# Performance work log

Hardware: AMD Instinct MI355X
Metric: run time of the kernel (lower is better)

The kernel has to match this reference:

```python
import jax, jax.numpy as jnp
import numpy as np

NR_EMB = 1024
B_COMMITMENT = 1.0


def setup_inputs() -> dict:
    key = jax.random.key(0)
    k1, k2 = jax.random.split(key)
    inpt = jax.random.normal(k1, (64, 2048, 64), dtype=jnp.float32)
    # VarianceScaling(uniform) over shape (D, K): limit = sqrt(3*scale/fan_in), scale=1, fan_in=D
    D = 64
    limit = np.sqrt(3.0 / D).astype(np.float32)
    emb_mtrx = jax.random.uniform(k2, (D, NR_EMB), dtype=jnp.float32, minval=-limit, maxval=limit)
    return {"inpt": inpt, "emb_mtrx": emb_mtrx}


def reference(inpt, emb_mtrx):
    D = inpt.shape[-1]
    x = inpt.reshape(-1, D)  # [N, D]
    dist = (jnp.sum(x * x, axis=1, keepdims=True)
            - 2.0 * (x @ emb_mtrx)
            + jnp.sum(emb_mtrx * emb_mtrx, axis=0, keepdims=True))
    idx = jnp.argmax(-dist, axis=1)  # [N]
    # avg_probs = mean of one-hot over N == normalized histogram (same math, no N x K one-hot)
    avg_probs = jnp.bincount(idx, length=NR_EMB).astype(inpt.dtype) / x.shape[0]
    perplexity = jnp.exp(-jnp.sum(avg_probs * jnp.log(avg_probs + 1e-10)))
    idx_nd = idx.reshape(inpt.shape[:-1])  # [B, T]
    q = jnp.take(emb_mtrx.T, idx_nd, axis=0)  # gather codebook rows -> [B, T, D]
    l_commitment = jnp.mean((jax.lax.stop_gradient(q) - inpt) ** 2)
    l_codebook = jnp.mean((q - jax.lax.stop_gradient(inpt)) ** 2)
    loss = B_COMMITMENT * l_commitment + l_codebook
    q = inpt + jax.lax.stop_gradient(q - inpt)  # straight-through estimator
    return q, loss, perplexity
```

## Files before the change

### kernel.cpp

```cpp
#include <hip/hip_runtime.h>

#define NROWS 131072
#define D 64
#define K 1024

typedef __attribute__((ext_vector_type(8))) short short8;
typedef __attribute__((ext_vector_type(4))) float f32x4;


__device__ __forceinline__ unsigned short f2bf(float f) {
    unsigned u = __float_as_uint(f);
    u += 0x7fff + ((u >> 16) & 1);
    return (unsigned short)(u >> 16);
}

__global__ __launch_bounds__(256) void prep_kernel(const float* __restrict__ E,
                                                   unsigned short* __restrict__ ehT,
                                                   float* __restrict__ eTf,
                                                   float* __restrict__ e2p,
                                                   int* __restrict__ hist) {
    const int k = (blockIdx.x & 3) * 256 + threadIdx.x;
    const int dq = blockIdx.x >> 2;
    float f[16];
    float s = 0.f;
#pragma unroll
    for (int j = 0; j < 16; ++j) {
        float v = E[(dq * 16 + j) * K + k];
        f[j] = v;
        s = fmaf(v, v, s);
    }
    short8 h0, h1;
#pragma unroll
    for (int j = 0; j < 8; ++j) {
        h0[j] = (short)f2bf(f[j]);
        h1[j] = (short)f2bf(f[8 + j]);
    }
    *(short8*)(ehT + (size_t)k * D + dq * 16) = h0;
    *(short8*)(ehT + (size_t)k * D + dq * 16 + 8) = h1;
#pragma unroll
    for (int c = 0; c < 4; ++c) {
        float4 v = {f[c * 4], f[c * 4 + 1], f[c * 4 + 2], f[c * 4 + 3]};
        *(float4*)(eTf + (size_t)k * D + dq * 16 + c * 4) = v;
    }
    e2p[dq * K + k] = s;
    if (dq == 0) hist[k] = 0;
}

__global__ __launch_bounds__(256, 4) void score_kernel(const float* __restrict__ X,
                                                       const unsigned short* __restrict__ ehT,
                                                       const float* __restrict__ e2p,
                                                       const float* __restrict__ eTf,
                                                       int* __restrict__ hist,
                                                       float* __restrict__ wavesum,
                                                       float* __restrict__ q) {
    __shared__ unsigned short ehs[256 * 64];
    __shared__ float e2s[256];
    __shared__ int idxs[4][32];

    const int wave = threadIdx.x >> 6;
    const int lane = threadIdx.x & 63;
    const int quad = lane >> 4;
    const int lc = lane & 15;
    const size_t row0 = (size_t)blockIdx.x * 128 + wave * 32;

    short8 ax[2][2];
#pragma unroll
    for (int s = 0; s < 2; ++s) {
        const float* xr = X + (row0 + s * 16 + lc) * D;
#pragma unroll
        for (int ks = 0; ks < 2; ++ks) {
            float4 a = *(const float4*)(xr + ks * 32 + quad * 8);
            float4 b = *(const float4*)(xr + ks * 32 + quad * 8 + 4);
            float f[8] = {a.x, a.y, a.z, a.w, b.x, b.y, b.z, b.w};
            short8 h;
#pragma unroll
            for (int j = 0; j < 8; ++j) h[j] = (short)f2bf(f[j]);
            ax[s][ks] = h;
        }
    }

    float best[2][4];
    int bidx[2][4];
#pragma unroll
    for (int s = 0; s < 2; ++s)
#pragma unroll
        for (int r = 0; r < 4; ++r) { best[s][r] = -3.4e38f; bidx[s][r] = 0; }

    const int boff0 = lc * 128 + ((quad ^ (lc & 7)) * 16);
    const int boff1 = lc * 128 + (((quad + 4) ^ (lc & 7)) * 16);

    for (int p = 0; p < 4; ++p) {
        if (p) __syncthreads();
#pragma unroll
        for (int r = 0; r < 8; ++r) {
            int slot = r * 256 + threadIdx.x;
            int c = slot >> 3;
            int o = slot & 7;
            short8 v = *(const short8*)(ehT + ((size_t)(p * 256 + c) * D + o * 8));
            *(short8*)((char*)ehs + c * 128 + ((o ^ (c & 7)) * 16)) = v;
        }
        if (threadIdx.x < 256) {
            int gk = p * 256 + threadIdx.x;
            e2s[threadIdx.x] = -0.5f * (e2p[gk] + e2p[K + gk] + e2p[2 * K + gk] + e2p[3 * K + gk]);
        }
        __syncthreads();

#pragma unroll 4
        for (int t = 0; t < 16; ++t) {
            const int cc = t * 16 + lc;
            const int code = p * 256 + cc;
            short8 eb0 = *(const short8*)((char*)ehs + t * 2048 + boff0);
            short8 eb1 = *(const short8*)((char*)ehs + t * 2048 + boff1);
            float ce2 = e2s[cc];
#pragma unroll
            for (int s = 0; s < 2; ++s) {
                f32x4 acc = {ce2, ce2, ce2, ce2};
                acc = __builtin_amdgcn_mfma_f32_16x16x32_bf16(ax[s][0], eb0, acc, 0, 0, 0);
                acc = __builtin_amdgcn_mfma_f32_16x16x32_bf16(ax[s][1], eb1, acc, 0, 0, 0);
#pragma unroll
                for (int r = 0; r < 4; ++r) {
                    if (acc[r] > best[s][r]) { best[s][r] = acc[r]; bidx[s][r] = code; }
                }
            }
        }
    }

#pragma unroll
    for (int off = 1; off <= 8; off <<= 1) {
#pragma unroll
        for (int s = 0; s < 2; ++s)
#pragma unroll
            for (int r = 0; r < 4; ++r) {
                float ob = __shfl_xor(best[s][r], off, 64);
                int oi = __shfl_xor(bidx[s][r], off, 64);
                if (ob > best[s][r] || (ob == best[s][r] && oi < bidx[s][r])) {
                    best[s][r] = ob;
                    bidx[s][r] = oi;
                }
            }
    }

    if (lc == 0) {
#pragma unroll
        for (int s = 0; s < 2; ++s)
#pragma unroll
            for (int r = 0; r < 4; ++r)
                idxs[wave][s * 16 + quad * 4 + r] = bidx[s][r];
    }
    if (lane < 32) atomicAdd(&hist[idxs[wave][lane]], 1);

    float ls = 0.f;
#pragma unroll 4
    for (int it = 0; it < 8; ++it) {
        int rl = it * 4 + quad;
        int k = idxs[wave][rl];
        size_t row = row0 + rl;
        float4 xv = *(const float4*)(X + row * D + lc * 4);
        float4 ev = *(const float4*)(eTf + (size_t)k * D + lc * 4);
        float4 o;
        float dx = ev.x - xv.x; ls = fmaf(dx, dx, ls); o.x = xv.x + dx;
        float dy = ev.y - xv.y; ls = fmaf(dy, dy, ls); o.y = xv.y + dy;
        float dz = ev.z - xv.z; ls = fmaf(dz, dz, ls); o.z = xv.z + dz;
        float dw = ev.w - xv.w; ls = fmaf(dw, dw, ls); o.w = xv.w + dw;
        *(float4*)(q + row * D + lc * 4) = o;
    }
    for (int off = 32; off > 0; off >>= 1) ls += __shfl_down(ls, off, 64);
    if (lane == 0) wavesum[blockIdx.x * 4 + wave] = ls;
}

__global__ __launch_bounds__(1024) void finalize_kernel(const int* __restrict__ hist,
                                                        const float* __restrict__ wavesum,
                                                        float* __restrict__ out) {
    __shared__ float redH[16], redL[16];
    int tid = threadIdx.x;
    float p = (float)hist[tid] * (1.0f / (float)NROWS);
    float term = p * logf(p + 1e-10f);
    float ls = wavesum[tid] + wavesum[tid + 1024] + wavesum[tid + 2048] + wavesum[tid + 3072];
    for (int off = 32; off > 0; off >>= 1) {
        term += __shfl_down(term, off, 64);
        ls += __shfl_down(ls, off, 64);
    }
    int lane = tid & 63, wid = tid >> 6;
    if (lane == 0) { redH[wid] = term; redL[wid] = ls; }
    __syncthreads();
    if (tid == 0) {
        float H = 0.f, L = 0.f;
#pragma unroll
        for (int i = 0; i < 16; ++i) { H += redH[i]; L += redL[i]; }
        out[(size_t)NROWS * D + 0] = 2.0f * (L / (float)(NROWS * D));
        out[(size_t)NROWS * D + 1] = expf(-H);
    }
}

extern "C" void kernel_launch(void* const* d_in, const int* in_sizes, int n_in,
                              void* d_out, int out_size, void* d_ws, size_t ws_size,
                              hipStream_t stream) {
    const float* X = (const float*)d_in[0];
    const float* E = (const float*)d_in[1];
    float* out = (float*)d_out;

    char* w = (char*)d_ws;
    unsigned short* ehT = (unsigned short*)(w + 0);
    float* eTf          = (float*)(w + 131072);
    float* e2p          = (float*)(w + 393216);
    int* hist           = (int*)(w + 409600);
    float* wavesum      = (float*)(w + 413696);

    prep_kernel<<<16, 256, 0, stream>>>(E, ehT, eTf, e2p, hist);
    score_kernel<<<NROWS / 128, 256, 0, stream>>>(X, ehT, e2p, eTf, hist, wavesum, out);
    finalize_kernel<<<1, 1024, 0, stream>>>(hist, wavesum, out);
}
```

Baseline: 134.4 us.

## Prefetch codebook tiles into registers and fold finalize into last block

The score kernel now loads the next 256-code bf16 codebook tile and its norm partials into registers while the current tile is being scored, so the global loads overlap with MFMA work instead of stalling each phase. The separate finalize kernel is removed: each block atomically adds its loss partial, and the last block (found with an atomic counter and thread fences) computes the perplexity and loss. This removes one kernel launch and the wavesum round trip, at the cost of more registers per thread (which may lower occupancy) and a global atomic per block.

After: 281.7 us. 110% more time.

```diff
diff --git a/kernel.cpp b/kernel.cpp
--- a/kernel.cpp
+++ b/kernel.cpp
@@ -18,7 +18,9 @@
                                                    unsigned short* __restrict__ ehT,
                                                    float* __restrict__ eTf,
                                                    float* __restrict__ e2p,
-                                                   int* __restrict__ hist) {
+                                                   int* __restrict__ hist,
+                                                   float* __restrict__ lacc,
+                                                   int* __restrict__ counter) {
     const int k = (blockIdx.x & 3) * 256 + threadIdx.x;
     const int dq = blockIdx.x >> 2;
     float f[16];
@@ -44,6 +46,7 @@
     }
     e2p[dq * K + k] = s;
     if (dq == 0) hist[k] = 0;
+    if (blockIdx.x == 0 && threadIdx.x == 0) { *lacc = 0.f; *counter = 0; }
 }
 
 __global__ __launch_bounds__(256, 4) void score_kernel(const float* __restrict__ X,
@@ -51,17 +54,31 @@
                                                        const float* __restrict__ e2p,
                                                        const float* __restrict__ eTf,
                                                        int* __restrict__ hist,
-                                                       float* __restrict__ wavesum,
+                                                       float* __restrict__ lacc,
+                                                       int* __restrict__ counter,
                                                        float* __restrict__ q) {
     __shared__ unsigned short ehs[256 * 64];
     __shared__ float e2s[256];
     __shared__ int idxs[4][32];
-
-    const int wave = threadIdx.x >> 6;
-    const int lane = threadIdx.x & 63;
+    __shared__ float red[4];
+    __shared__ int amLast;
+
+    const int tid = threadIdx.x;
+    const int wave = tid >> 6;
+    const int lane = tid & 63;
     const int quad = lane >> 4;
     const int lc = lane & 15;
     const size_t row0 = (size_t)blockIdx.x * 128 + wave * 32;
+
+    const int so = tid & 7;
+
+    short8 pf[8];
+#pragma unroll
+    for (int r = 0; r < 8; ++r) {
+        int c = (r * 256 + tid) >> 3;
+        pf[r] = *(const short8*)(ehT + ((size_t)c * D + so * 8));
+    }
+    float e2a = e2p[tid], e2b = e2p[K + tid], e2c_ = e2p[2 * K + tid], e2d = e2p[3 * K + tid];
 
     short8 ax[2][2];
 #pragma unroll
@@ -93,15 +110,18 @@
         if (p) __syncthreads();
 #pragma unroll
         for (int r = 0; r < 8; ++r) {
-            int slot = r * 256 + threadIdx.x;
-            int c = slot >> 3;
-            int o = slot & 7;
-            short8 v = *(const short8*)(ehT + ((size_t)(p * 256 + c) * D + o * 8));
-            *(short8*)((char*)ehs + c * 128 + ((o ^ (c & 7)) * 16)) = v;
-        }
-        if (threadIdx.x < 256) {
-            int gk = p * 256 + threadIdx.x;
-            e2s[threadIdx.x] = -0.5f * (e2p[gk] + e2p[K + gk] + e2p[2 * K + gk] + e2p[3 * K + gk]);
+            int c = (r * 256 + tid) >> 3;
+            *(short8*)((char*)ehs + c * 128 + ((so ^ (c & 7)) * 16)) = pf[r];
+        }
+        e2s[tid] = -0.5f * (e2a + e2b + e2c_ + e2d);
+        if (p < 3) {
+#pragma unroll
+            for (int r = 0; r < 8; ++r) {
+                int c = (r * 256 + tid) >> 3;
+                pf[r] = *(const short8*)(ehT + ((size_t)((p + 1) * 256 + c) * D + so * 8));
+            }
+            int gk = (p + 1) * 256 + tid;
+            e2a = e2p[gk]; e2b = e2p[K + gk]; e2c_ = e2p[2 * K + gk]; e2d = e2p[3 * K + gk];
         }
         __syncthreads();
 
@@ -165,30 +185,32 @@
         *(float4*)(q + row * D + lc * 4) = o;
     }
     for (int off = 32; off > 0; off >>= 1) ls += __shfl_down(ls, off, 64);
-    if (lane == 0) wavesum[blockIdx.x * 4 + wave] = ls;
-}
-
-__global__ __launch_bounds__(1024) void finalize_kernel(const int* __restrict__ hist,
-                                                        const float* __restrict__ wavesum,
-                                                        float* __restrict__ out) {
-    __shared__ float redH[16], redL[16];
-    int tid = threadIdx.x;
-    float p = (float)hist[tid] * (1.0f / (float)NROWS);
-    float term = p * logf(p + 1e-10f);
-    float ls = wavesum[tid] + wavesum[tid + 1024] + wavesum[tid + 2048] + wavesum[tid + 3072];
-    for (int off = 32; off > 0; off >>= 1) {
-        term += __shfl_down(term, off, 64);
-        ls += __shfl_down(ls, off, 64);
-    }
-    int lane = tid & 63, wid = tid >> 6;
-    if (lane == 0) { redH[wid] = term; redL[wid] = ls; }
+    if (lane == 0) red[wave] = ls;
     __syncthreads();
-    if (tid == 0) {
-        float H = 0.f, L = 0.f;
-#pragma unroll
-        for (int i = 0; i < 16; ++i) { H += redH[i]; L += redL[i]; }
-        out[(size_t)NROWS * D + 0] = 2.0f * (L / (float)(NROWS * D));
-        out[(size_t)NROWS * D + 1] = expf(-H);
+    if (tid == 0) atomicAdd(lacc, red[0] + red[1] + red[2] + red[3]);
+
+    __threadfence();
+    if (tid == 0) amLast = (atomicAdd(counter, 1) == (int)gridDim.x - 1);
+    __syncthreads();
+    if (amLast) {
+        __threadfence();
+        float term = 0.f;
+#pragma unroll
+        for (int j = 0; j < 4; ++j) {
+            int c = atomicAdd(&hist[tid + j * 256], 0);
+            float pp = (float)c * (1.0f / (float)NROWS);
+            term += pp * logf(pp + 1e-10f);
+        }
+        for (int off = 32; off > 0; off >>= 1) term += __shfl_down(term, off, 64);
+        if (lane == 0) red[wave] = term;
+        __syncthreads();
+        if (tid == 0) {
+            float H = red[0] + red[1] + red[2] + red[3];
+            float L = atomicAdd(lacc, 0.f);
+            float* out = q;
+            out[(size_t)NROWS * D + 0] = 2.0f * (L / (float)(NROWS * D));
+            out[(size_t)NROWS * D + 1] = expf(-H);
+        }
     }
 }
 
@@ -204,9 +226,9 @@
     float* eTf          = (float*)(w + 131072);
     float* e2p          = (float*)(w + 393216);
     int* hist           = (int*)(w + 409600);
-    float* wavesum      = (float*)(w + 413696);
-
-    prep_kernel<<<16, 256, 0, stream>>>(E, ehT, eTf, e2p, hist);
-    score_kernel<<<NROWS / 128, 256, 0, stream>>>(X, ehT, e2p, eTf, hist, wavesum, out);
-    finalize_kernel<<<1, 1024, 0, stream>>>(hist, wavesum, out);
-}
+    float* lacc         = (float*)(w + 413696);
+    int* counter        = (int*)(w + 413700);
+
+    prep_kernel<<<16, 256, 0, stream>>>(E, ehT, eTf, e2p, hist, lacc, counter);
+    score_kernel<<<NROWS / 128, 256, 0, stream>>>(X, ehT, e2p, eTf, hist, lacc, counter, out);
+}
```
